# Kernel optimization log

Measured on AMD Instinct MI355X. Metric: run time of the kernel, lower is better.

## Reference

```python
import jax, jax.numpy as jnp
import numpy as np


def setup_inputs() -> dict:
    key = jax.random.key(0)
    ks = jax.random.split(key, 9)
    B, C, H, W = 4, 256, 64, 64
    Ci = C // 2
    s = 0.05  # keep activations numerically tame
    return {
        "x": jax.random.normal(ks[0], (B, C, H, W), jnp.float32),
        "w_g": jax.random.normal(ks[1], (Ci, C), jnp.float32) * s,
        "b_g": jax.random.normal(ks[2], (Ci,), jnp.float32) * s,
        "w_theta": jax.random.normal(ks[3], (Ci, C), jnp.float32) * s,
        "b_theta": jax.random.normal(ks[4], (Ci,), jnp.float32) * s,
        "w_phi": jax.random.normal(ks[5], (Ci, C), jnp.float32) * s,
        "b_phi": jax.random.normal(ks[6], (Ci,), jnp.float32) * s,
        "w_out": jax.random.normal(ks[7], (C, Ci), jnp.float32) * s,
        "b_out": jax.random.normal(ks[8], (C,), jnp.float32) * s,
    }


def reference(x, w_g, b_g, w_theta, b_theta, w_phi, b_phi, w_out, b_out):
    B, C, H, W = x.shape
    Ci = w_g.shape[0]
    N = H * W
    xr = x.reshape(B, C, N)  # flatten spatial dims

    def proj(w, b):  # 1x1 conv == per-pixel GEMM
        return jnp.einsum("oc,bcn->bon", w, xr) + b[None, :, None]

    g_x = proj(w_g, b_g)          # [B, Ci, N]
    theta_x = proj(w_theta, b_theta)
    phi_x = proj(w_phi, b_phi)

    scale = jnp.asarray(Ci, x.dtype) ** 0.5
    f = jnp.einsum("bci,bcj->bij", theta_x, phi_x) / scale  # [B, N, N]
    attn = jax.nn.softmax(f, axis=-1)

    # out[b,c,i] = sum_j g_x[b,c,j] * attn[b,i,j]
    out = jnp.einsum("bcj,bij->bci", g_x, attn)             # [B, Ci, N]
    y = jnp.einsum("oc,bcn->bon", w_out, out) + b_out[None, :, None]
    return y.reshape(B, C, H, W) + x
```

## Files before the change

### kernel.cpp

```cpp
#include <hip/hip_runtime.h>
#include <hip/hip_bf16.h>


typedef float f32x4 __attribute__((ext_vector_type(4)));
typedef float f32x16 __attribute__((ext_vector_type(16)));
typedef short s16x8 __attribute__((ext_vector_type(8)));
typedef short s16x4 __attribute__((ext_vector_type(4)));

#define B_  4
#define C_  256
#define CI_ 128
#define N_  4096

#define OFF_Q    (8ull  << 20)
#define OFF_K    (12ull << 20)
#define OFF_G    (16ull << 20)
#define OFF_O    (20ull << 20)
#define OFF_WQK  (24ull << 20)
#define OFF_WG   (OFF_WQK + 131072)
#define OFF_WOUT (OFF_WG  + 65536)
#define OFF_BQK  (OFF_WOUT + 65536)
#define OFF_BG   (OFF_BQK + 1024)
#define OFF_BOUT (OFF_BG  + 512)
#define OFF_END  (OFF_BOUT + 1024)

__device__ inline f32x4 mfma16(s16x8 a, s16x8 b, f32x4 c) {
    return __builtin_amdgcn_mfma_f32_16x16x32_bf16(a, b, c, 0, 0, 0);
}
__device__ inline f32x16 mfma32(s16x8 a, s16x8 b, f32x16 c) {
    return __builtin_amdgcn_mfma_f32_32x32x16_bf16(a, b, c, 0, 0, 0);
}
__device__ inline s16x8 ld8(const __hip_bfloat16* p) { return *(const s16x8*)p; }
__device__ inline float b2f(short u) {
    return __uint_as_float(((unsigned int)(unsigned short)u) << 16);
}
__device__ inline unsigned int pk2(float a, float b) {
    __hip_bfloat162 h;
    h.x = __float2bfloat16(a); h.y = __float2bfloat16(b);
    return *(unsigned int*)&h;
}
__device__ inline void gload_lds16(const void* g, void* l) {
    __builtin_amdgcn_global_load_lds(
        (const __attribute__((address_space(1))) unsigned int*)g,
        (__attribute__((address_space(3))) unsigned int*)l, 16, 0, 0);
}
__device__ inline float fexp2(float x) { return __builtin_amdgcn_exp2f(x); }

__global__ void prep_weights(const float* wg, const float* bg,
                             const float* wt, const float* bt,
                             const float* wp, const float* bp,
                             const float* wo, const float* bo, char* ws) {
    __hip_bfloat16* Wqk  = (__hip_bfloat16*)(ws + OFF_WQK);
    __hip_bfloat16* Wg   = (__hip_bfloat16*)(ws + OFF_WG);
    __hip_bfloat16* Wout = (__hip_bfloat16*)(ws + OFF_WOUT);
    float* Bqk  = (float*)(ws + OFF_BQK);
    float* Bg   = (float*)(ws + OFF_BG);
    float* Bout = (float*)(ws + OFF_BOUT);
    const float rs = 0.08838834764831845f * 1.4426950408889634f;
    int idx = blockIdx.x * 256 + threadIdx.x;
    if (idx < 65536) {
        int r = idx >> 8, c = idx & 255;
        float v = (r < 128) ? wt[r * 256 + c] * rs : wp[(r - 128) * 256 + c];
        Wqk[idx] = __float2bfloat16(v);
    }
    if (idx < 32768) {
        Wg[idx]   = __float2bfloat16(wg[idx]);
        Wout[idx] = __float2bfloat16(wo[idx]);
    }
    if (idx < 256) { Bqk[idx] = (idx < 128) ? bt[idx] * rs : bp[idx - 128]; Bout[idx] = bo[idx]; }
    if (idx < 128) Bg[idx] = bg[idx];
}

__global__ __launch_bounds__(256) void proj(const float* x, char* ws) {
    const __hip_bfloat16* Wqk = (const __hip_bfloat16*)(ws + OFF_WQK);
    const __hip_bfloat16* Wg  = (const __hip_bfloat16*)(ws + OFF_WG);
    const float* Bqk = (const float*)(ws + OFF_BQK);
    const float* Bg  = (const float*)(ws + OFF_BG);
    __hip_bfloat16* Q  = (__hip_bfloat16*)(ws + OFF_Q);
    __hip_bfloat16* Kb = (__hip_bfloat16*)(ws + OFF_K);
    __hip_bfloat16* G  = (__hip_bfloat16*)(ws + OFF_G);

    __shared__ char at[32 * 512];

    int b = blockIdx.y, n0 = blockIdx.x * 32;
    int t = threadIdx.x;
    int w = t >> 6, l = t & 63, lr = l & 15, lg = l >> 4;

    {
        int n4 = (t & 7) * 4;
        int cp = t >> 3;
        const float* xb = x + ((size_t)b * C_) * N_ + n0 + n4;
#pragma unroll
        for (int p = 0; p < 4; p++) {
            int c0 = (p * 32 + cp) * 2;
            f32x4 vA = *(const f32x4*)(xb + (size_t)c0 * N_);
            f32x4 vB = *(const f32x4*)(xb + (size_t)(c0 + 1) * N_);
            int slot = c0 >> 3, coff = (c0 & 7) << 1;
#pragma unroll
            for (int i = 0; i < 4; i++) {
                int n = n4 + i;
                *(unsigned int*)(&at[n * 512 + ((slot ^ (n & 7)) << 4) + coff]) =
                    pk2(vA[i], vB[i]);
            }
        }
    }
    __syncthreads();

    f32x4 acc[4][2] = {};
    f32x4 accg[2][2] = {};
    int o0q = w * 64, o0g = w * 32;
#pragma unroll
    for (int kk = 0; kk < 8; kk++) {
        s16x8 a[2];
#pragma unroll
        for (int nf = 0; nf < 2; nf++) {
            int row = nf * 16 + lr;
            int s = (4 * kk + lg) ^ (row & 7);
            a[nf] = *(const s16x8*)(&at[row * 512 + s * 16]);
        }
#pragma unroll
        for (int of = 0; of < 4; of++) {
            s16x8 bb = ld8(Wqk + (size_t)(o0q + 16 * of + lr) * C_ + kk * 32 + lg * 8);
            acc[of][0] = mfma16(a[0], bb, acc[of][0]);
            acc[of][1] = mfma16(a[1], bb, acc[of][1]);
        }
#pragma unroll
        for (int og = 0; og < 2; og++) {
            s16x8 ag = ld8(Wg + (size_t)(o0g + 16 * og + lr) * C_ + kk * 32 + lg * 8);
            accg[og][0] = mfma16(ag, a[0], accg[og][0]);
            accg[og][1] = mfma16(ag, a[1], accg[og][1]);
        }
    }
#pragma unroll
    for (int of = 0; of < 4; of++) {
        int o = o0q + 16 * of + lr;
        float bias = Bqk[o];
#pragma unroll
        for (int nf = 0; nf < 2; nf++) {
#pragma unroll
            for (int i = 0; i < 4; i++) {
                int n = n0 + 16 * nf + lg * 4 + i;
                float v = acc[of][nf][i] + bias;
                if (o < 128) Q [(size_t)(b * N_ + n) * CI_ + o]         = __float2bfloat16(v);
                else         Kb[(size_t)(b * N_ + n) * CI_ + (o - 128)] = __float2bfloat16(v);
            }
        }
    }
#pragma unroll
    for (int og = 0; og < 2; og++) {
#pragma unroll
        for (int i = 0; i < 4; i++) {
            int o = o0g + 16 * og + lg * 4 + i;
            float bias = Bg[o];
#pragma unroll
            for (int nf = 0; nf < 2; nf++) {
                int n = n0 + 16 * nf + lr;
                G[(size_t)(b * CI_ + o) * N_ + n] = __float2bfloat16(accg[og][nf][i] + bias);
            }
        }
    }
}

__global__ __launch_bounds__(256, 3) void flash9(char* ws, int nchunk,
                                                 unsigned long long off_part,
                                                 unsigned long long off_ml) {
    const __hip_bfloat16* Q  = (const __hip_bfloat16*)(ws + OFF_Q);
    const __hip_bfloat16* Kb = (const __hip_bfloat16*)(ws + OFF_K);
    const __hip_bfloat16* G  = (const __hip_bfloat16*)(ws + OFF_G);
    __hip_bfloat16* OP = (__hip_bfloat16*)(ws + off_part);
    float* ML = (float*)(ws + off_ml);

    __shared__ char kbuf[2][32 * 256];
    __shared__ char vbuf[2][128 * 64];

    int L = blockIdx.x;
    int npairs = B_ * nchunk;
    int pair = L % npairs, qt = L / npairs;
    int b = pair / nchunk, cz = pair % nchunk;
    int per = 128 / nchunk, rem = 128 % nchunk;
    int jb_t = per * cz + (cz < rem ? cz : rem);
    int sz_t = per + (cz < rem ? 1 : 0);
    int jb = jb_t << 5, je = jb + (sz_t << 5);

    int w = threadIdx.x >> 6, l = threadIdx.x & 63;
    int cl = l & 31, hi = l >> 5;
    int q0 = qt * 128 + w * 32;
    int kkey = (l & 7) << 4;
    int vkey = (l >> 1) & 3;

    auto STAGE = [&](int pb_, int j0_) {
#pragma unroll
        for (int i = 0; i < 2; i++) {
            int row = w * 8 + i * 4 + (l >> 4);
            int bcol = ((l & 15) << 4) ^ ((row & 7) << 4);
            const char* src = (const char*)Kb + (((size_t)b * N_ + j0_ + row) << 8) + bcol;
            gload_lds16(src, &kbuf[pb_][(w * 8 + i * 4) * 256]);
        }
#pragma unroll
        for (int i = 0; i < 2; i++) {
            int c = w * 32 + i * 16 + (l >> 2);
            int srcslot = (l & 3) ^ ((l >> 3) & 3);
            const char* src = (const char*)G + ((((size_t)b * CI_ + c) * N_ + j0_) << 1)
                              + (srcslot << 4);
            gload_lds16(src, &vbuf[pb_][(w * 32 + i * 16) * 64]);
        }
    };

    s16x8 qb[8];
    {
        const __hip_bfloat16* qrow = Q + ((size_t)b * N_ + q0 + cl) * CI_ + hi * 8;
#pragma unroll
        for (int st = 0; st < 8; st++) qb[st] = ld8(qrow + st * 16);
    }

    f32x16 oacc[4] = {};
    float m_i = 0.f, lsum = 0.f;

    STAGE(0, jb);
    __syncthreads();
    int pb = 0;

    for (int j0 = jb; j0 < je; j0 += 32) {
        if (j0 + 32 < je) STAGE(pb ^ 1, j0 + 32);
        const char* kb = kbuf[pb];
        const char* vbb = vbuf[pb];
        f32x16 s = {};
        __builtin_amdgcn_s_setprio(1);
#pragma unroll
        for (int st = 0; st < 8; st++) {
            s16x8 kf = *(const s16x8*)(kb + cl * 256 + ((((st << 1) + hi) << 4) ^ kkey));
            s = mfma32(kf, qb[st], s);
        }
        __builtin_amdgcn_s_setprio(0);
        if (j0 == jb) {
            float t0 = fmaxf(fmaxf(s[0], s[1]), fmaxf(s[2], s[3]));
            float t1 = fmaxf(fmaxf(s[4], s[5]), fmaxf(s[6], s[7]));
            float t2 = fmaxf(fmaxf(s[8], s[9]), fmaxf(s[10], s[11]));
            float t3 = fmaxf(fmaxf(s[12], s[13]), fmaxf(s[14], s[15]));
            float tm = fmaxf(fmaxf(t0, t1), fmaxf(t2, t3));
            tm = fmaxf(tm, __shfl_xor(tm, 32));
            m_i = tm;
        }
#pragma unroll
        for (int r = 0; r < 16; r++) s[r] = fexp2(s[r] - m_i);
        lsum += ((s[0] + s[1]) + (s[2] + s[3])) + ((s[4] + s[5]) + (s[6] + s[7]))
              + ((s[8] + s[9]) + (s[10] + s[11])) + ((s[12] + s[13]) + (s[14] + s[15]));
        union { unsigned int u[4]; s16x8 v; } pa0, pa1;
#pragma unroll
        for (int i = 0; i < 4; i++) {
            pa0.u[i] = pk2(s[2 * i], s[2 * i + 1]);
            pa1.u[i] = pk2(s[8 + 2 * i], s[9 + 2 * i]);
        }
        __builtin_amdgcn_s_setprio(1);
#pragma unroll
        for (int u = 0; u < 2; u++) {
            s16x8 pa = u ? pa1.v : pa0.v;
#pragma unroll
            for (int cb = 0; cb < 4; cb++) {
                const char* base = vbb + ((cb * 32 + cl) << 6) + hi * 8;
                union { s16x4 h[2]; s16x8 v; } vf;
                vf.h[0] = *(const s16x4*)(base + ((((u << 1))     ^ vkey) << 4));
                vf.h[1] = *(const s16x4*)(base + ((((u << 1) | 1) ^ vkey) << 4));
                oacc[cb] = mfma32(pa, vf.v, oacc[cb]);
            }
        }
        __builtin_amdgcn_s_setprio(0);
        __syncthreads();
        pb ^= 1;
    }
    lsum += __shfl_xor(lsum, 32);
#pragma unroll
    for (int cb = 0; cb < 4; cb++) {
#pragma unroll
        for (int r = 0; r < 16; r++) {
            int q = q0 + (r & 3) + 8 * (r >> 2) + 4 * hi;
            OP[((size_t)(cz * B_ + b) * N_ + q) * CI_ + cb * 32 + cl] =
                __float2bfloat16(oacc[cb][r]);
        }
    }
    if (l < 32) {
        size_t mi = ((size_t)(cz * B_ + b) * N_ + q0 + l) * 2;
        ML[mi] = m_i;
        ML[mi + 1] = lsum;
    }
}

template <int NC>
__global__ __launch_bounds__(256) void combine(char* ws,
                                               unsigned long long off_part,
                                               unsigned long long off_ml) {
    const __hip_bfloat16* OP = (const __hip_bfloat16*)(ws + off_part);
    const float* ML = (const float*)(ws + off_ml);
    __hip_bfloat16* O = (__hip_bfloat16*)(ws + OFF_O);
    int idx = blockIdx.x * 256 + threadIdx.x;
    int cg = idx & 15, n = (idx >> 4) & (N_ - 1), b = idx >> 16;
    float mz[NC], lz[NC], M = -1e30f;
#pragma unroll
    for (int z = 0; z < NC; z++) {
        size_t mi = ((size_t)(z * B_ + b) * N_ + n) * 2;
        mz[z] = ML[mi]; lz[z] = ML[mi + 1];
        M = fmaxf(M, mz[z]);
    }
    float Lsum = 0.f, wz[NC];
#pragma unroll
    for (int z = 0; z < NC; z++) { wz[z] = fexp2(mz[z] - M); Lsum += lz[z] * wz[z]; }
    float inv = 1.f / Lsum;
    float o[8] = {};
#pragma unroll
    for (int z = 0; z < NC; z++) {
        s16x8 v = ld8(OP + ((size_t)(z * B_ + b) * N_ + n) * CI_ + cg * 8);
        float wv = wz[z] * inv;
#pragma unroll
        for (int i = 0; i < 8; i++) o[i] += wv * b2f(v[i]);
    }
    s16x8 r;
#pragma unroll
    for (int i = 0; i < 8; i++) {
        __hip_bfloat16 h = __float2bfloat16(o[i]);
        r[i] = *(short*)&h;
    }
    *(s16x8*)(O + ((size_t)b * N_ + n) * CI_ + cg * 8) = r;
}

__global__ __launch_bounds__(256) void gemm_out(const float* x, char* ws, float* y) {
    const __hip_bfloat16* Ob = (const __hip_bfloat16*)(ws + OFF_O);
    const __hip_bfloat16* Wo = (const __hip_bfloat16*)(ws + OFF_WOUT);
    const float* Bout = (const float*)(ws + OFF_BOUT);
    int b = blockIdx.y;
    int w = threadIdx.x >> 6, l = threadIdx.x & 63, lr = l & 15, lg = l >> 4;
    int n0 = blockIdx.x * 32;
    int o0 = w * 64;
    f32x4 acc[4][2] = {};
#pragma unroll
    for (int kk = 0; kk < 4; kk++) {
        s16x8 bb[2];
#pragma unroll
        for (int nf = 0; nf < 2; nf++)
            bb[nf] = ld8(Ob + (size_t)(b * N_ + n0 + 16 * nf + lr) * CI_ + kk * 32 + lg * 8);
#pragma unroll
        for (int of = 0; of < 4; of++) {
            s16x8 a = ld8(Wo + (size_t)(o0 + 16 * of + lr) * CI_ + kk * 32 + lg * 8);
#pragma unroll
            for (int nf = 0; nf < 2; nf++)
                acc[of][nf] = mfma16(a, bb[nf], acc[of][nf]);
        }
    }
#pragma unroll
    for (int of = 0; of < 4; of++) {
#pragma unroll
        for (int i = 0; i < 4; i++) {
            int o = o0 + 16 * of + lg * 4 + i;
            float bias = Bout[o];
#pragma unroll
            for (int nf = 0; nf < 2; nf++) {
                int n = n0 + 16 * nf + lr;
                size_t idx = (size_t)(b * C_ + o) * N_ + n;
                y[idx] = acc[of][nf][i] + bias + x[idx];
            }
        }
    }
}

extern "C" void kernel_launch(void* const* d_in, const int* in_sizes, int n_in,
                              void* d_out, int out_size, void* d_ws, size_t ws_size,
                              hipStream_t stream) {
    const float* x  = (const float*)d_in[0];
    const float* wg = (const float*)d_in[1];
    const float* bg = (const float*)d_in[2];
    const float* wt = (const float*)d_in[3];
    const float* bt = (const float*)d_in[4];
    const float* wp = (const float*)d_in[5];
    const float* bp = (const float*)d_in[6];
    const float* wo = (const float*)d_in[7];
    const float* bo = (const float*)d_in[8];
    char* ws = (char*)d_ws;
    float* y = (float*)d_out;

    unsigned long long need6 = OFF_END + (24ull << 20) + (1ull << 20);
    unsigned long long need4 = OFF_END + (16ull << 20) + (1ull << 20);
    int nchunk;
    unsigned long long off_part, off_ml;
    if (ws_size >= need6) {
        nchunk = 6; off_part = OFF_END; off_ml = OFF_END + (24ull << 20);
    } else if (ws_size >= need4) {
        nchunk = 4; off_part = OFF_END; off_ml = OFF_END + (16ull << 20);
    } else {
        nchunk = 2; off_part = 0ull; off_ml = OFF_END;
    }

    prep_weights<<<256, 256, 0, stream>>>(wg, bg, wt, bt, wp, bp, wo, bo, ws);
    proj<<<dim3(128, 4), 256, 0, stream>>>(x, ws);
    flash9<<<dim3(32 * B_ * nchunk), 256, 0, stream>>>(ws, nchunk, off_part, off_ml);
    if (nchunk == 6)      combine<6><<<1024, 256, 0, stream>>>(ws, off_part, off_ml);
    else if (nchunk == 4) combine<4><<<1024, 256, 0, stream>>>(ws, off_part, off_ml);
    else                  combine<2><<<1024, 256, 0, stream>>>(ws, off_part, off_ml);
    gemm_out<<<dim3(128, 4), 256, 0, stream>>>(x, ws, y);
}
```

Baseline: 94.78 us.

## Compute QK^T in FP8 with pre-tiled K layout and more key chunks

Q and K are now emitted in FP8 (e4m3) by the projection kernel, with Q pre-scaled by 16 to use the FP8 dynamic range. K is written in a 32-key tile layout so the attention kernel stages it with one contiguous LDS load per wave. The score GEMM uses the 32x32x16 fp8 MFMA, and the scale is undone inside the exp2 via an FMA. The key split rises from 6 to 8 chunks with a higher occupancy bound. This halves Q/K bandwidth and LDS traffic for the score GEMM at the cost of reduced precision in the attention logits.

```diff
diff --git a/kernel.cpp b/kernel.cpp
--- a/kernel.cpp
+++ b/kernel.cpp
@@ -30,6 +30,9 @@
 __device__ inline f32x16 mfma32(s16x8 a, s16x8 b, f32x16 c) {
     return __builtin_amdgcn_mfma_f32_32x32x16_bf16(a, b, c, 0, 0, 0);
 }
+__device__ inline f32x16 mfma32f8(long a, long b, f32x16 c) {
+    return __builtin_amdgcn_mfma_f32_32x32x16_fp8_fp8(a, b, c, 0, 0, 0);
+}
 __device__ inline s16x8 ld8(const __hip_bfloat16* p) { return *(const s16x8*)p; }
 __device__ inline float b2f(short u) {
     return __uint_as_float(((unsigned int)(unsigned short)u) << 16);
@@ -38,6 +41,10 @@
     __hip_bfloat162 h;
     h.x = __float2bfloat16(a); h.y = __float2bfloat16(b);
     return *(unsigned int*)&h;
+}
+__device__ inline unsigned char f2fp8(float v) {
+    int r = __builtin_amdgcn_cvt_pk_fp8_f32(v, v, 0, false);
+    return (unsigned char)(r & 0xff);
 }
 __device__ inline void gload_lds16(const void* g, void* l) {
     __builtin_amdgcn_global_load_lds(
@@ -56,18 +63,18 @@
     float* Bqk  = (float*)(ws + OFF_BQK);
     float* Bg   = (float*)(ws + OFF_BG);
     float* Bout = (float*)(ws + OFF_BOUT);
-    const float rs = 0.08838834764831845f * 1.4426950408889634f;
+    const float rs16 = 0.08838834764831845f * 1.4426950408889634f * 16.0f;
     int idx = blockIdx.x * 256 + threadIdx.x;
     if (idx < 65536) {
         int r = idx >> 8, c = idx & 255;
-        float v = (r < 128) ? wt[r * 256 + c] * rs : wp[(r - 128) * 256 + c];
+        float v = (r < 128) ? wt[r * 256 + c] * rs16 : wp[(r - 128) * 256 + c];
         Wqk[idx] = __float2bfloat16(v);
     }
     if (idx < 32768) {
         Wg[idx]   = __float2bfloat16(wg[idx]);
         Wout[idx] = __float2bfloat16(wo[idx]);
     }
-    if (idx < 256) { Bqk[idx] = (idx < 128) ? bt[idx] * rs : bp[idx - 128]; Bout[idx] = bo[idx]; }
+    if (idx < 256) { Bqk[idx] = (idx < 128) ? bt[idx] * rs16 : bp[idx - 128]; Bout[idx] = bo[idx]; }
     if (idx < 128) Bg[idx] = bg[idx];
 }
 
@@ -76,9 +83,9 @@
     const __hip_bfloat16* Wg  = (const __hip_bfloat16*)(ws + OFF_WG);
     const float* Bqk = (const float*)(ws + OFF_BQK);
     const float* Bg  = (const float*)(ws + OFF_BG);
-    __hip_bfloat16* Q  = (__hip_bfloat16*)(ws + OFF_Q);
-    __hip_bfloat16* Kb = (__hip_bfloat16*)(ws + OFF_K);
-    __hip_bfloat16* G  = (__hip_bfloat16*)(ws + OFF_G);
+    unsigned char* Qf = (unsigned char*)(ws + OFF_Q);
+    unsigned char* Kt = (unsigned char*)(ws + OFF_K);
+    __hip_bfloat16* G = (__hip_bfloat16*)(ws + OFF_G);
 
     __shared__ char at[32 * 512];
 
@@ -141,8 +148,15 @@
             for (int i = 0; i < 4; i++) {
                 int n = n0 + 16 * nf + lg * 4 + i;
                 float v = acc[of][nf][i] + bias;
-                if (o < 128) Q [(size_t)(b * N_ + n) * CI_ + o]         = __float2bfloat16(v);
-                else         Kb[(size_t)(b * N_ + n) * CI_ + (o - 128)] = __float2bfloat16(v);
+                unsigned char u8 = f2fp8(v);
+                if (o < 128) {
+                    Qf[((size_t)b * N_ + n) * 128 + o] = u8;
+                } else {
+                    int op = o - 128;
+                    size_t a2 = (((size_t)b * (N_ / 32) + (n >> 5)) << 12) +
+                                ((op >> 3) << 8) + ((n & 31) << 3) + (op & 7);
+                    Kt[a2] = u8;
+                }
             }
         }
     }
@@ -161,16 +175,16 @@
     }
 }
 
-__global__ __launch_bounds__(256, 3) void flash9(char* ws, int nchunk,
-                                                 unsigned long long off_part,
-                                                 unsigned long long off_ml) {
-    const __hip_bfloat16* Q  = (const __hip_bfloat16*)(ws + OFF_Q);
-    const __hip_bfloat16* Kb = (const __hip_bfloat16*)(ws + OFF_K);
-    const __hip_bfloat16* G  = (const __hip_bfloat16*)(ws + OFF_G);
+__global__ __launch_bounds__(256, 4) void flashf8(char* ws, int nchunk,
+                                                  unsigned long long off_part,
+                                                  unsigned long long off_ml) {
+    const unsigned char* Qf = (const unsigned char*)(ws + OFF_Q);
+    const unsigned char* Kt = (const unsigned char*)(ws + OFF_K);
+    const __hip_bfloat16* G = (const __hip_bfloat16*)(ws + OFF_G);
     __hip_bfloat16* OP = (__hip_bfloat16*)(ws + off_part);
     float* ML = (float*)(ws + off_ml);
 
-    __shared__ char kbuf[2][32 * 256];
+    __shared__ char kbuf[2][4096];
     __shared__ char vbuf[2][128 * 64];
 
     int L = blockIdx.x;
@@ -185,16 +199,13 @@
     int w = threadIdx.x >> 6, l = threadIdx.x & 63;
     int cl = l & 31, hi = l >> 5;
     int q0 = qt * 128 + w * 32;
-    int kkey = (l & 7) << 4;
     int vkey = (l >> 1) & 3;
 
     auto STAGE = [&](int pb_, int j0_) {
-#pragma unroll
-        for (int i = 0; i < 2; i++) {
-            int row = w * 8 + i * 4 + (l >> 4);
-            int bcol = ((l & 15) << 4) ^ ((row & 7) << 4);
-            const char* src = (const char*)Kb + (((size_t)b * N_ + j0_ + row) << 8) + bcol;
-            gload_lds16(src, &kbuf[pb_][(w * 8 + i * 4) * 256]);
+        {
+            const char* src = (const char*)Kt +
+                (((size_t)b * (N_ / 32) + (j0_ >> 5)) << 12) + w * 1024 + (l << 4);
+            gload_lds16(src, &kbuf[pb_][w * 1024]);
         }
 #pragma unroll
         for (int i = 0; i < 2; i++) {
@@ -206,15 +217,15 @@
         }
     };
 
-    s16x8 qb[8];
+    long qf[8];
     {
-        const __hip_bfloat16* qrow = Q + ((size_t)b * N_ + q0 + cl) * CI_ + hi * 8;
-#pragma unroll
-        for (int st = 0; st < 8; st++) qb[st] = ld8(qrow + st * 16);
+        const char* qrow = (const char*)Qf + ((size_t)b * N_ + q0 + cl) * 128 + hi * 8;
+#pragma unroll
+        for (int st = 0; st < 8; st++) qf[st] = *(const long*)(qrow + st * 16);
     }
 
     f32x16 oacc[4] = {};
-    float m_i = 0.f, lsum = 0.f;
+    float m_i = 0.f, lsum = 0.f, negmc = 0.f;
 
     STAGE(0, jb);
     __syncthreads();
@@ -228,8 +239,8 @@
         __builtin_amdgcn_s_setprio(1);
 #pragma unroll
         for (int st = 0; st < 8; st++) {
-            s16x8 kf = *(const s16x8*)(kb + cl * 256 + ((((st << 1) + hi) << 4) ^ kkey));
-            s = mfma32(kf, qb[st], s);
+            long kf = *(const long*)(kb + (((st << 1) + hi) << 8) + (cl << 3));
+            s = mfma32f8(kf, qf[st], s);
         }
         __builtin_amdgcn_s_setprio(0);
         if (j0 == jb) {
@@ -240,9 +251,10 @@
             float tm = fmaxf(fmaxf(t0, t1), fmaxf(t2, t3));
             tm = fmaxf(tm, __shfl_xor(tm, 32));
             m_i = tm;
-        }
-#pragma unroll
-        for (int r = 0; r < 16; r++) s[r] = fexp2(s[r] - m_i);
+            negmc = -m_i * 0.0625f;
+        }
+#pragma unroll
+        for (int r = 0; r < 16; r++) s[r] = fexp2(fmaf(s[r], 0.0625f, negmc));
         lsum += ((s[0] + s[1]) + (s[2] + s[3])) + ((s[4] + s[5]) + (s[6] + s[7]))
               + ((s[8] + s[9]) + (s[10] + s[11])) + ((s[12] + s[13]) + (s[14] + s[15]));
         union { unsigned int u[4]; s16x8 v; } pa0, pa1;
@@ -280,7 +292,7 @@
     }
     if (l < 32) {
         size_t mi = ((size_t)(cz * B_ + b) * N_ + q0 + l) * 2;
-        ML[mi] = m_i;
+        ML[mi] = m_i * 0.0625f;
         ML[mi + 1] = lsum;
     }
 }
@@ -376,12 +388,12 @@
     char* ws = (char*)d_ws;
     float* y = (float*)d_out;
 
-    unsigned long long need6 = OFF_END + (24ull << 20) + (1ull << 20);
+    unsigned long long need8 = OFF_END + (32ull << 20) + (2ull << 20);
     unsigned long long need4 = OFF_END + (16ull << 20) + (1ull << 20);
     int nchunk;
     unsigned long long off_part, off_ml;
-    if (ws_size >= need6) {
-        nchunk = 6; off_part = OFF_END; off_ml = OFF_END + (24ull << 20);
+    if (ws_size >= need8) {
+        nchunk = 8; off_part = OFF_END; off_ml = OFF_END + (32ull << 20);
     } else if (ws_size >= need4) {
         nchunk = 4; off_part = OFF_END; off_ml = OFF_END + (16ull << 20);
     } else {
@@ -390,8 +402,8 @@
 
     prep_weights<<<256, 256, 0, stream>>>(wg, bg, wt, bt, wp, bp, wo, bo, ws);
     proj<<<dim3(128, 4), 256, 0, stream>>>(x, ws);
-    flash9<<<dim3(32 * B_ * nchunk), 256, 0, stream>>>(ws, nchunk, off_part, off_ml);
-    if (nchunk == 6)      combine<6><<<1024, 256, 0, stream>>>(ws, off_part, off_ml);
+    flashf8<<<dim3(32 * B_ * nchunk), 256, 0, stream>>>(ws, nchunk, off_part, off_ml);
+    if (nchunk == 8)      combine<8><<<1024, 256, 0, stream>>>(ws, off_part, off_ml);
     else if (nchunk == 4) combine<4><<<1024, 256, 0, stream>>>(ws, off_part, off_ml);
     else                  combine<2><<<1024, 256, 0, stream>>>(ws, off_part, off_ml);
     gemm_out<<<dim3(128, 4), 256, 0, stream>>>(x, ws, y);
```

Measured after the change: 91.12 us. 3.9% less time.
